# Kernel optimization log

Hardware: AMD Instinct MI355X
Metric: run time of the kernel (lower is better)

## Reference

```python
import jax, jax.numpy as jnp
import numpy as np

H = 32
W = 32
HIDDEN = 64
NUM_CLASSES = 10
BATCH = 128


def setup_inputs() -> dict:
    key = jax.random.key(0)
    ks = jax.random.split(key, 5)
    D = 4 * HIDDEN * H * W  # number_of_output_dimensions()
    return {
        "x": jax.random.normal(ks[0], (BATCH, 1, H, W), jnp.float32),
        "w_in": jax.random.normal(ks[1], (HIDDEN, 1), jnp.float32) * 0.1,
        "b_in": jnp.zeros((HIDDEN,), jnp.float32),
        "w_state": jax.random.normal(ks[2], (HIDDEN, HIDDEN, 2), jnp.float32) * (1.0 / np.sqrt(2 * HIDDEN)),
        "b_state": jnp.zeros((HIDDEN,), jnp.float32),
        "w_fc": jax.random.normal(ks[3], (D, NUM_CLASSES), jnp.float32) * 0.01,
        "b_fc": jnp.zeros((NUM_CLASSES,), jnp.float32),
    }


def _skew(x):
    # x: [B,1,H,W] -> [B,1,H,W+H-1]; row r shifted right by r (diagonal skew)
    Ws = W + H - 1
    col = jnp.arange(Ws)[None, :] - jnp.arange(H)[:, None]  # [H,Ws]
    valid = ((col >= 0) & (col < W)).astype(x.dtype)
    colc = jnp.clip(col, 0, W - 1)
    rows = jnp.arange(H)[:, None]
    return x[:, :, rows, colc] * valid[None, None]


def _one_direction(x, w_in, b_in, w_state, b_state):
    # Diagonal-scan MDRNN over skewed columns.
    B = x.shape[0]
    xs = _skew(x)  # [B,1,H,Ws]
    # Input projection for all columns at once (1x1 conv equivalent)
    xin = jnp.einsum('oc,bchw->bohw', w_in, xs) + b_in[None, :, None, None]
    cols = jnp.moveaxis(xin, 3, 0)  # [Ws,B,HIDDEN,H]

    w_up, w_same = w_state[:, :, 0], w_state[:, :, 1]

    def step(h, xc):
        # conv1d(kernel=2, padding=1) over column, bottom padding removed:
        # out[r] = w_up @ h[r-1] + w_same @ h[r]
        h_up = jnp.pad(h, ((0, 0), (0, 0), (1, 0)))[:, :, :H]
        s = (jnp.einsum('oi,bir->bor', w_up, h_up)
             + jnp.einsum('oi,bir->bor', w_same, h)
             + b_state[None, :, None])
        hn = jnp.tanh(s + xc)
        return hn, hn

    h0 = jnp.zeros((B, HIDDEN, H), x.dtype)
    _, ys = jax.lax.scan(step, h0, cols)  # [Ws,B,HIDDEN,H]
    acts = jnp.moveaxis(ys, 0, 3)  # [B,HIDDEN,H,Ws]
    # Unskew: out[..., r, c] = acts[..., r, c + r]
    ccols = jnp.arange(W)[None, :] + jnp.arange(H)[:, None]  # [H,W]
    rows = jnp.arange(H)[:, None]
    return acts[:, :, rows, ccols]  # [B,HIDDEN,H,W]


def reference(x, w_in, b_in, w_state, b_state, w_fc, b_fc):
    B = x.shape[0]
    # Four scanning directions via flips on dims 2 and 3, concatenated on batch
    x2 = x[:, :, ::-1, :]
    x3 = x[:, :, :, ::-1]
    x4 = x[:, :, ::-1, ::-1]
    xm = jnp.concatenate([x, x2, x3, x4], axis=0)  # [4B,1,H,W]
    acts = _one_direction(xm, w_in, b_in, w_state, b_state)  # [4B,HIDDEN,H,W]
    # index_select interleaving: example b gets its 4 direction copies contiguously
    sel = (jnp.arange(B)[:, None] + B * jnp.arange(4)[None, :]).reshape(-1)
    a = acts[sel].reshape(B, -1)  # [B, 4*HIDDEN*H*W]
    logits = a @ w_fc + b_fc
    return jax.nn.log_softmax(logits, axis=-1)
```

## Files before the change

kernel.cpp:

```cpp
#include <hip/hip_runtime.h>
#include <hip/hip_bf16.h>

#define NHID 64
#define NT   63
#define NBD  512
#define HLDS_STR 72
#define XSTR 35

typedef __attribute__((ext_vector_type(8))) short bf16x8;
typedef __attribute__((ext_vector_type(4))) float f32x4;

__device__ __forceinline__ float tanh_fast(float x) {
    const float e = __expf(2.0f * x);
    const float r = __builtin_amdgcn_rcpf(e + 1.0f);
    return 1.0f - 2.0f * r;
}

__device__ __forceinline__ unsigned int cvt_pk_bf16(float lo, float hi) {
    unsigned int r;
    asm("v_cvt_pk_bf16_f32 %0, %1, %2" : "=v"(r) : "v"(lo), "v"(hi));
    return r;
}

__device__ __forceinline__ float bf2f(unsigned int u16) {
    return __uint_as_float(u16 << 16);
}

#define SKEW_R0(t)  ((t) > 31 ? (t) - 31 : 0)
#define SKEW_R1(t)  ((t) < 31 ? (t) : 31)
#define SKEW_OFF(t) ((t) < 32 ? ((t) * ((t) + 1)) >> 1 : 1024 - (((63 - (t)) * (64 - (t))) >> 1))

#define LGKM_BARRIER() do {                                   \
    asm volatile("s_waitcnt lgkmcnt(0)" ::: "memory");        \
    __builtin_amdgcn_s_barrier();                             \
    asm volatile("" ::: "memory");                            \
} while (0)

__global__ __launch_bounds__(512, 4) void k_rnn(
    const float* __restrict__ x,
    const float* __restrict__ w_in,
    const float* __restrict__ b_in,
    const float* __restrict__ w_state,
    const float* __restrict__ b_state,
    unsigned short* __restrict__ acts_c)
{
    __shared__ __align__(16) unsigned short h0buf[33 * HLDS_STR];
    __shared__ __align__(16) unsigned short h1buf[33 * HLDS_STR];
    __shared__ float xs[32 * XSTR];

    const int tid = threadIdx.x;
    const int bd  = blockIdx.x;
    const int d   = bd >> 7;
    const int b   = bd & 127;
    const int lane = tid & 63;
    const int wave = tid >> 6;
    const int wo = wave >> 1;
    const int wr = wave & 1;
    const int n  = lane & 15;
    const int g  = lane >> 4;

    const bool flr = (d & 1) != 0;
    const bool flc = (d & 2) != 0;
    const float* xb = x + (size_t)b * 1024;
    for (int idx = tid; idx < 1024; idx += 512) {
        const int r = idx >> 5, c = idx & 31;
        xs[r * XSTR + c] = xb[(flr ? 31 - r : r) * 32 + (flc ? 31 - c : c)];
    }

    for (int m2 = tid; m2 < (33 * HLDS_STR) / 2; m2 += 512) {
        ((unsigned int*)h0buf)[m2] = 0u;
        ((unsigned int*)h1buf)[m2] = 0u;
    }

    bf16x8 a_hi[4], a_lo[4];
    {
        const int o_a = wo * 16 + n;
        #pragma unroll
        for (int kt = 0; kt < 4; ++kt) {
            const int s  = kt >> 1;
            const int cb = (kt & 1) * 32 + g * 8;
            bf16x8 hi8, lo8;
            #pragma unroll
            for (int j = 0; j < 8; ++j) {
                const float w = w_state[((size_t)o_a * 64 + cb + j) * 2 + s];
                const unsigned int hp = cvt_pk_bf16(w, 0.0f);
                const float wh = bf2f(hp & 0xffffu);
                const unsigned int lp = cvt_pk_bf16(w - wh, 0.0f);
                hi8[j] = (short)(hp & 0xffffu);
                lo8[j] = (short)(lp & 0xffffu);
            }
            a_hi[kt] = hi8;
            a_lo[kt] = lo8;
        }
    }

    float biasr[4], winr[4];
    #pragma unroll
    for (int j = 0; j < 4; ++j) {
        const int o = wo * 16 + g * 4 + j;
        biasr[j] = b_in[o] + b_state[o];
        winr[j]  = w_in[o];
    }

    const int r_out = wr * 16 + n;
    const int rdoff = r_out * HLDS_STR + g * 8;
    const int wroff = (r_out + 1) * HLDS_STR;
    const int cb0 = wo * 16 + g * 4;
    const int tlo = wr * 16;
    const float* xs_r = &xs[r_out * XSTR];

    const bool flusher = tid < 256;
    const int r_f = tid >> 3;
    const int sc  = (tid & 7) * 8;
    const int fl_off = (r_f + 1) * HLDS_STR + sc;
    unsigned short* actp = acts_c + (size_t)bd * 65536 + (size_t)r_f * 1984 + sc;

    __syncthreads();

#define STEP(T, RB, WB) do {                                                    \
    if ((unsigned)((T) - tlo) < 48u) {                                          \
        const bf16x8 b0 = *(const bf16x8*)&RB[rdoff];                           \
        const bf16x8 b1 = *(const bf16x8*)&RB[rdoff + 32];                      \
        const bf16x8 b2 = *(const bf16x8*)&RB[rdoff + HLDS_STR];                \
        const bf16x8 b3 = *(const bf16x8*)&RB[rdoff + HLDS_STR + 32];           \
        f32x4 ah = {0,0,0,0}, al = {0,0,0,0};                                   \
        ah = __builtin_amdgcn_mfma_f32_16x16x32_bf16(a_hi[0], b0, ah, 0,0,0);   \
        al = __builtin_amdgcn_mfma_f32_16x16x32_bf16(a_lo[0], b0, al, 0,0,0);   \
        ah = __builtin_amdgcn_mfma_f32_16x16x32_bf16(a_hi[1], b1, ah, 0,0,0);   \
        al = __builtin_amdgcn_mfma_f32_16x16x32_bf16(a_lo[1], b1, al, 0,0,0);   \
        ah = __builtin_amdgcn_mfma_f32_16x16x32_bf16(a_hi[2], b2, ah, 0,0,0);   \
        al = __builtin_amdgcn_mfma_f32_16x16x32_bf16(a_lo[2], b2, al, 0,0,0);   \
        ah = __builtin_amdgcn_mfma_f32_16x16x32_bf16(a_hi[3], b3, ah, 0,0,0);   \
        al = __builtin_amdgcn_mfma_f32_16x16x32_bf16(a_lo[3], b3, al, 0,0,0);   \
        const int c_ = (T) - r_out;                                             \
        const float xv = ((unsigned)c_ < 32u) ? xs_r[c_ & 31] : 0.0f;           \
        const float h0 = tanh_fast(ah[0] + al[0] + biasr[0] + winr[0] * xv);    \
        const float h1 = tanh_fast(ah[1] + al[1] + biasr[1] + winr[1] * xv);    \
        const float h2 = tanh_fast(ah[2] + al[2] + biasr[2] + winr[2] * xv);    \
        const float h3 = tanh_fast(ah[3] + al[3] + biasr[3] + winr[3] * xv);    \
        uint2 pk; pk.x = cvt_pk_bf16(h0, h1); pk.y = cvt_pk_bf16(h2, h3);       \
        *(uint2*)&WB[wroff + cb0] = pk;                                         \
    }                                                                           \
    LGKM_BARRIER();                                                             \
    if (flusher) {                                                              \
        const uint4 av = *(const uint4*)&WB[fl_off];                            \
        if ((unsigned)((T) - r_f) < 32u) *(uint4*)actp = av;                    \
        actp += 64;                                                             \
    }                                                                           \
} while (0)

    for (int sp = 0; sp < 31; ++sp) {
        const int t = 2 * sp;
        STEP(t,     h0buf, h1buf);
        STEP(t + 1, h1buf, h0buf);
    }
    STEP(62, h0buf, h1buf);
#undef STEP
}

__global__ __launch_bounds__(256) void k_prep(
    const float* __restrict__ w_fc,
    unsigned short* __restrict__ wt_swz)
{
    const int t = blockIdx.y;
    const int tid = threadIdx.x;
    const int r0 = SKEW_R0(t), r1 = SKEW_R1(t);
    const int cnt = r1 - r0 + 1;
    const int span = cnt << 10;
    int f = blockIdx.x * 2048 + tid * 8;
    const int fdst = f;
    if (f >= 4 * span) return;
    int d = 0;
    while (f >= span) { f -= span; ++d; }
    const int ks   = f >> 9;
    const int lane = (f >> 3) & 63;
    const int g = lane >> 4, n = lane & 15;
    unsigned int pk[4];
    #pragma unroll
    for (int jj = 0; jj < 4; ++jj) {
        float v[2] = {0.0f, 0.0f};
        #pragma unroll
        for (int h = 0; h < 2; ++h) {
            const int j = jj * 2 + h;
            const int k = ks * 32 + g * 8 + j;
            const int r = r0 + (k >> 6);
            const int o = k & 63;
            const int c = t - r;
            if (n < 10)
                v[h] = w_fc[((((size_t)(d * 64 + o)) << 10) + (r << 5) + c) * 10 + n];
        }
        pk[jj] = cvt_pk_bf16(v[0], v[1]);
    }
    uint4 st; st.x = pk[0]; st.y = pk[1]; st.z = pk[2]; st.w = pk[3];
    *(uint4*)(wt_swz + (size_t)SKEW_OFF(t) * 4096 + fdst) = st;
}

__global__ __launch_bounds__(256, 4) void k_fc(
    const unsigned short* __restrict__ acts_c,
    const unsigned short* __restrict__ wt_swz,
    float* __restrict__ partial)
{
    const int tid = threadIdx.x;
    const int blk = blockIdx.x;
    const int t   = blk >> 3;
    const int d   = (blk >> 1) & 3;
    const int mh  = blk & 1;
    const int lane = tid & 63;
    const int wv  = tid >> 6;
    const int g   = lane >> 4;
    const int n   = lane & 15;

    const int r0 = SKEW_R0(t), r1 = SKEW_R1(t);
    const int cnt = r1 - r0 + 1;
    const int off = SKEW_OFF(t);

    const int tb = d * 128 + mh * 64 + wv * 16;
    const unsigned short* Ap = acts_c + (size_t)(tb + n) * 65536
                             + (size_t)r0 * 1984 + (size_t)t * 64 + g * 8;
    const unsigned short* Bp = wt_swz
        + ((size_t)off * 4 + (size_t)d * cnt) * 1024 + lane * 8;

    f32x4 acc = {0.f, 0.f, 0.f, 0.f};
    #pragma unroll 2
    for (int q = 0; q < cnt; ++q) {
        const bf16x8 a0  = *(const bf16x8*)(Ap);
        const bf16x8 bb0 = *(const bf16x8*)(Bp);
        const bf16x8 a1  = *(const bf16x8*)(Ap + 32);
        const bf16x8 bb1 = *(const bf16x8*)(Bp + 512);
        acc = __builtin_amdgcn_mfma_f32_16x16x32_bf16(a0, bb0, acc, 0, 0, 0);
        acc = __builtin_amdgcn_mfma_f32_16x16x32_bf16(a1, bb1, acc, 0, 0, 0);
        Ap += 1984;
        Bp += 1024;
    }
    const int batch = tb + g * 4;
    #pragma unroll
    for (int reg = 0; reg < 4; ++reg)
        partial[((size_t)t * 512 + batch + reg) * 16 + n] = acc[reg];
}

__global__ __launch_bounds__(256) void k_out(
    const float* __restrict__ partial,
    const float* __restrict__ b_fc,
    float* __restrict__ out)
{
    __shared__ float lred[252 * 10];
    __shared__ float lgs[10];
    __shared__ float lse;
    const int b = blockIdx.x;
    const int tid = threadIdx.x;
    if (tid < 252) {
        const int t = tid >> 2, d = tid & 3;
        const float* p = partial + ((size_t)t * 512 + d * 128 + b) * 16;
        #pragma unroll
        for (int n2 = 0; n2 < 10; ++n2) lred[tid * 10 + n2] = p[n2];
    }
    __syncthreads();
    if (tid < 10) {
        float s = b_fc[tid];
        for (int i = 0; i < 252; ++i) s += lred[i * 10 + tid];
        lgs[tid] = s;
    }
    __syncthreads();
    if (tid == 0) {
        float m = lgs[0];
        for (int nn = 1; nn < 10; ++nn) m = fmaxf(m, lgs[nn]);
        float ssum = 0.0f;
        for (int nn = 0; nn < 10; ++nn) ssum += __expf(lgs[nn] - m);
        lse = m + __logf(ssum);
    }
    __syncthreads();
    if (tid < 10) out[b * 10 + tid] = lgs[tid] - lse;
}

extern "C" void kernel_launch(void* const* d_in, const int* in_sizes, int n_in,
                              void* d_out, int out_size, void* d_ws, size_t ws_size,
                              hipStream_t stream)
{
    const float* x       = (const float*)d_in[0];
    const float* w_in    = (const float*)d_in[1];
    const float* b_in    = (const float*)d_in[2];
    const float* w_state = (const float*)d_in[3];
    const float* b_state = (const float*)d_in[4];
    const float* w_fc    = (const float*)d_in[5];
    const float* b_fc    = (const float*)d_in[6];
    float* out = (float*)d_out;

    unsigned short* wt_swz = (unsigned short*)d_ws;
    float* partial = (float*)((char*)d_ws + (size_t)(8u << 20));
    unsigned short* acts_c = (unsigned short*)((char*)d_ws + (size_t)(16u << 20));

    k_prep<<<dim3(64, 63), 256, 0, stream>>>(w_fc, wt_swz);
    k_rnn <<<512, 512, 0, stream>>>(x, w_in, b_in, w_state, b_state, acts_c);
    k_fc  <<<504, 256, 0, stream>>>(acts_c, wt_swz, partial);
    k_out <<<128, 256, 0, stream>>>(partial, b_fc, out);
}
```

Baseline: 74.28 us.

## Fuse w_fc prep into RNN kernel, drop split-bf16 weights, halve RNN block size

Merges the w_fc swizzle/prep kernel into the RNN kernel as extra blocks, which removes one launch and lets the prep work overlap with the recurrence. The RNN weights now use a single bf16 copy instead of a hi/lo split, halving the MFMA count per step at some cost in accuracy. Each block drops from 512 to 256 threads, with every wave computing two output tiles, and activations go straight from registers to global memory instead of through a separate flush phase after the barrier.

```diff
diff --git a/kernel.cpp b/kernel.cpp
--- a/kernel.cpp
+++ b/kernel.cpp
@@ -36,84 +36,117 @@
     asm volatile("" ::: "memory");                            \
 } while (0)
 
-__global__ __launch_bounds__(512, 4) void k_rnn(
+__global__ __launch_bounds__(256, 4) void k_main(
     const float* __restrict__ x,
     const float* __restrict__ w_in,
     const float* __restrict__ b_in,
     const float* __restrict__ w_state,
     const float* __restrict__ b_state,
-    unsigned short* __restrict__ acts_c)
+    unsigned short* __restrict__ acts_c,
+    const float* __restrict__ w_fc,
+    unsigned short* __restrict__ wt_swz)
 {
     __shared__ __align__(16) unsigned short h0buf[33 * HLDS_STR];
     __shared__ __align__(16) unsigned short h1buf[33 * HLDS_STR];
     __shared__ float xs[32 * XSTR];
 
     const int tid = threadIdx.x;
+
+    if (blockIdx.x >= 512) {
+        const int rel = blockIdx.x - 512;
+        const int t   = rel >> 6;
+        const int sub = rel & 63;
+        const int r0 = SKEW_R0(t), r1 = SKEW_R1(t);
+        const int cnt = r1 - r0 + 1;
+        const int span = cnt << 10;
+        int f = sub * 2048 + tid * 8;
+        const int fdst = f;
+        if (f >= 4 * span) return;
+        int d = 0;
+        while (f >= span) { f -= span; ++d; }
+        const int ks   = f >> 9;
+        const int lane = (f >> 3) & 63;
+        const int g = lane >> 4, n = lane & 15;
+        unsigned int pk[4];
+        #pragma unroll
+        for (int jj = 0; jj < 4; ++jj) {
+            float v[2] = {0.0f, 0.0f};
+            #pragma unroll
+            for (int h = 0; h < 2; ++h) {
+                const int j = jj * 2 + h;
+                const int k = ks * 32 + g * 8 + j;
+                const int r = r0 + (k >> 6);
+                const int o = k & 63;
+                const int c = t - r;
+                if (n < 10)
+                    v[h] = w_fc[((((size_t)(d * 64 + o)) << 10) + (r << 5) + c) * 10 + n];
+            }
+            pk[jj] = cvt_pk_bf16(v[0], v[1]);
+        }
+        uint4 st; st.x = pk[0]; st.y = pk[1]; st.z = pk[2]; st.w = pk[3];
+        *(uint4*)(wt_swz + (size_t)SKEW_OFF(t) * 4096 + fdst) = st;
+        return;
+    }
+
     const int bd  = blockIdx.x;
     const int d   = bd >> 7;
     const int b   = bd & 127;
     const int lane = tid & 63;
     const int wave = tid >> 6;
-    const int wo = wave >> 1;
-    const int wr = wave & 1;
+    const int wp = wave & 1;
+    const int nt = wave >> 1;
     const int n  = lane & 15;
     const int g  = lane >> 4;
 
     const bool flr = (d & 1) != 0;
     const bool flc = (d & 2) != 0;
     const float* xb = x + (size_t)b * 1024;
-    for (int idx = tid; idx < 1024; idx += 512) {
+    for (int idx = tid; idx < 1024; idx += 256) {
         const int r = idx >> 5, c = idx & 31;
         xs[r * XSTR + c] = xb[(flr ? 31 - r : r) * 32 + (flc ? 31 - c : c)];
     }
 
-    for (int m2 = tid; m2 < (33 * HLDS_STR) / 2; m2 += 512) {
+    for (int m2 = tid; m2 < (33 * HLDS_STR) / 2; m2 += 256) {
         ((unsigned int*)h0buf)[m2] = 0u;
         ((unsigned int*)h1buf)[m2] = 0u;
     }
 
-    bf16x8 a_hi[4], a_lo[4];
-    {
-        const int o_a = wo * 16 + n;
+    bf16x8 a0[4], a1[4];
+    #pragma unroll
+    for (int wl = 0; wl < 2; ++wl) {
+        const int o = wp * 32 + wl * 16 + n;
         #pragma unroll
         for (int kt = 0; kt < 4; ++kt) {
             const int s  = kt >> 1;
             const int cb = (kt & 1) * 32 + g * 8;
-            bf16x8 hi8, lo8;
+            bf16x8 w8;
             #pragma unroll
             for (int j = 0; j < 8; ++j) {
-                const float w = w_state[((size_t)o_a * 64 + cb + j) * 2 + s];
-                const unsigned int hp = cvt_pk_bf16(w, 0.0f);
-                const float wh = bf2f(hp & 0xffffu);
-                const unsigned int lp = cvt_pk_bf16(w - wh, 0.0f);
-                hi8[j] = (short)(hp & 0xffffu);
-                lo8[j] = (short)(lp & 0xffffu);
+                const float w = w_state[((size_t)o * 64 + cb + j) * 2 + s];
+                w8[j] = (short)(cvt_pk_bf16(w, 0.0f) & 0xffffu);
             }
-            a_hi[kt] = hi8;
-            a_lo[kt] = lo8;
+            if (wl == 0) a0[kt] = w8; else a1[kt] = w8;
         }
     }
 
-    float biasr[4], winr[4];
+    float biasr[2][4], winr[2][4];
     #pragma unroll
-    for (int j = 0; j < 4; ++j) {
-        const int o = wo * 16 + g * 4 + j;
-        biasr[j] = b_in[o] + b_state[o];
-        winr[j]  = w_in[o];
-    }
-
-    const int r_out = wr * 16 + n;
+    for (int wl = 0; wl < 2; ++wl)
+        #pragma unroll
+        for (int j = 0; j < 4; ++j) {
+            const int o = wp * 32 + wl * 16 + g * 4 + j;
+            biasr[wl][j] = b_in[o] + b_state[o];
+            winr[wl][j]  = w_in[o];
+        }
+
+    const int r_out = nt * 16 + n;
     const int rdoff = r_out * HLDS_STR + g * 8;
     const int wroff = (r_out + 1) * HLDS_STR;
-    const int cb0 = wo * 16 + g * 4;
-    const int tlo = wr * 16;
+    const int cb0 = wp * 32 + g * 4;
+    const int tlo = nt * 16;
     const float* xs_r = &xs[r_out * XSTR];
 
-    const bool flusher = tid < 256;
-    const int r_f = tid >> 3;
-    const int sc  = (tid & 7) * 8;
-    const int fl_off = (r_f + 1) * HLDS_STR + sc;
-    unsigned short* actp = acts_c + (size_t)bd * 65536 + (size_t)r_f * 1984 + sc;
+    unsigned short* actp = acts_c + (size_t)bd * 65536 + (size_t)r_out * 1984 + cb0;
 
     __syncthreads();
 
@@ -123,30 +156,42 @@
         const bf16x8 b1 = *(const bf16x8*)&RB[rdoff + 32];                      \
         const bf16x8 b2 = *(const bf16x8*)&RB[rdoff + HLDS_STR];                \
         const bf16x8 b3 = *(const bf16x8*)&RB[rdoff + HLDS_STR + 32];           \
-        f32x4 ah = {0,0,0,0}, al = {0,0,0,0};                                   \
-        ah = __builtin_amdgcn_mfma_f32_16x16x32_bf16(a_hi[0], b0, ah, 0,0,0);   \
-        al = __builtin_amdgcn_mfma_f32_16x16x32_bf16(a_lo[0], b0, al, 0,0,0);   \
-        ah = __builtin_amdgcn_mfma_f32_16x16x32_bf16(a_hi[1], b1, ah, 0,0,0);   \
-        al = __builtin_amdgcn_mfma_f32_16x16x32_bf16(a_lo[1], b1, al, 0,0,0);   \
-        ah = __builtin_amdgcn_mfma_f32_16x16x32_bf16(a_hi[2], b2, ah, 0,0,0);   \
-        al = __builtin_amdgcn_mfma_f32_16x16x32_bf16(a_lo[2], b2, al, 0,0,0);   \
-        ah = __builtin_amdgcn_mfma_f32_16x16x32_bf16(a_hi[3], b3, ah, 0,0,0);   \
-        al = __builtin_amdgcn_mfma_f32_16x16x32_bf16(a_lo[3], b3, al, 0,0,0);   \
+        f32x4 s0a = {0,0,0,0}, s0b = {0,0,0,0};                                 \
+        f32x4 s1a = {0,0,0,0}, s1b = {0,0,0,0};                                 \
+        s0a = __builtin_amdgcn_mfma_f32_16x16x32_bf16(a0[0], b0, s0a, 0,0,0);   \
+        s1a = __builtin_amdgcn_mfma_f32_16x16x32_bf16(a1[0], b0, s1a, 0,0,0);   \
+        s0b = __builtin_amdgcn_mfma_f32_16x16x32_bf16(a0[2], b2, s0b, 0,0,0);   \
+        s1b = __builtin_amdgcn_mfma_f32_16x16x32_bf16(a1[2], b2, s1b, 0,0,0);   \
+        s0a = __builtin_amdgcn_mfma_f32_16x16x32_bf16(a0[1], b1, s0a, 0,0,0);   \
+        s1a = __builtin_amdgcn_mfma_f32_16x16x32_bf16(a1[1], b1, s1a, 0,0,0);   \
+        s0b = __builtin_amdgcn_mfma_f32_16x16x32_bf16(a0[3], b3, s0b, 0,0,0);   \
+        s1b = __builtin_amdgcn_mfma_f32_16x16x32_bf16(a1[3], b3, s1b, 0,0,0);   \
         const int c_ = (T) - r_out;                                             \
         const float xv = ((unsigned)c_ < 32u) ? xs_r[c_ & 31] : 0.0f;           \
-        const float h0 = tanh_fast(ah[0] + al[0] + biasr[0] + winr[0] * xv);    \
-        const float h1 = tanh_fast(ah[1] + al[1] + biasr[1] + winr[1] * xv);    \
-        const float h2 = tanh_fast(ah[2] + al[2] + biasr[2] + winr[2] * xv);    \
-        const float h3 = tanh_fast(ah[3] + al[3] + biasr[3] + winr[3] * xv);    \
-        uint2 pk; pk.x = cvt_pk_bf16(h0, h1); pk.y = cvt_pk_bf16(h2, h3);       \
-        *(uint2*)&WB[wroff + cb0] = pk;                                         \
+        uint2 pk0, pk1;                                                         \
+        {                                                                       \
+            const float h0 = tanh_fast(s0a[0] + s0b[0] + biasr[0][0] + winr[0][0] * xv); \
+            const float h1 = tanh_fast(s0a[1] + s0b[1] + biasr[0][1] + winr[0][1] * xv); \
+            const float h2 = tanh_fast(s0a[2] + s0b[2] + biasr[0][2] + winr[0][2] * xv); \
+            const float h3 = tanh_fast(s0a[3] + s0b[3] + biasr[0][3] + winr[0][3] * xv); \
+            pk0.x = cvt_pk_bf16(h0, h1); pk0.y = cvt_pk_bf16(h2, h3);           \
+            *(uint2*)&WB[wroff + cb0] = pk0;                                    \
+        }                                                                       \
+        {                                                                       \
+            const float h0 = tanh_fast(s1a[0] + s1b[0] + biasr[1][0] + winr[1][0] * xv); \
+            const float h1 = tanh_fast(s1a[1] + s1b[1] + biasr[1][1] + winr[1][1] * xv); \
+            const float h2 = tanh_fast(s1a[2] + s1b[2] + biasr[1][2] + winr[1][2] * xv); \
+            const float h3 = tanh_fast(s1a[3] + s1b[3] + biasr[1][3] + winr[1][3] * xv); \
+            pk1.x = cvt_pk_bf16(h0, h1); pk1.y = cvt_pk_bf16(h2, h3);           \
+            *(uint2*)&WB[wroff + cb0 + 16] = pk1;                               \
+        }                                                                       \
+        if ((unsigned)c_ < 32u) {                                               \
+            *(uint2*)(actp)      = pk0;                                         \
+            *(uint2*)(actp + 16) = pk1;                                         \
+        }                                                                       \
     }                                                                           \
     LGKM_BARRIER();                                                             \
-    if (flusher) {                                                              \
-        const uint4 av = *(const uint4*)&WB[fl_off];                            \
-        if ((unsigned)((T) - r_f) < 32u) *(uint4*)actp = av;                    \
-        actp += 64;                                                             \
-    }                                                                           \
+    actp += 64;                                                                 \
 } while (0)
 
     for (int sp = 0; sp < 31; ++sp) {
@@ -156,43 +201,6 @@
     }
     STEP(62, h0buf, h1buf);
 #undef STEP
-}
-
-__global__ __launch_bounds__(256) void k_prep(
-    const float* __restrict__ w_fc,
-    unsigned short* __restrict__ wt_swz)
-{
-    const int t = blockIdx.y;
-    const int tid = threadIdx.x;
-    const int r0 = SKEW_R0(t), r1 = SKEW_R1(t);
-    const int cnt = r1 - r0 + 1;
-    const int span = cnt << 10;
-    int f = blockIdx.x * 2048 + tid * 8;
-    const int fdst = f;
-    if (f >= 4 * span) return;
-    int d = 0;
-    while (f >= span) { f -= span; ++d; }
-    const int ks   = f >> 9;
-    const int lane = (f >> 3) & 63;
-    const int g = lane >> 4, n = lane & 15;
-    unsigned int pk[4];
-    #pragma unroll
-    for (int jj = 0; jj < 4; ++jj) {
-        float v[2] = {0.0f, 0.0f};
-        #pragma unroll
-        for (int h = 0; h < 2; ++h) {
-            const int j = jj * 2 + h;
-            const int k = ks * 32 + g * 8 + j;
-            const int r = r0 + (k >> 6);
-            const int o = k & 63;
-            const int c = t - r;
-            if (n < 10)
-                v[h] = w_fc[((((size_t)(d * 64 + o)) << 10) + (r << 5) + c) * 10 + n];
-        }
-        pk[jj] = cvt_pk_bf16(v[0], v[1]);
-    }
-    uint4 st; st.x = pk[0]; st.y = pk[1]; st.z = pk[2]; st.w = pk[3];
-    *(uint4*)(wt_swz + (size_t)SKEW_OFF(t) * 4096 + fdst) = st;
 }
 
 __global__ __launch_bounds__(256, 4) void k_fc(
@@ -289,8 +297,8 @@
     float* partial = (float*)((char*)d_ws + (size_t)(8u << 20));
     unsigned short* acts_c = (unsigned short*)((char*)d_ws + (size_t)(16u << 20));
 
-    k_prep<<<dim3(64, 63), 256, 0, stream>>>(w_fc, wt_swz);
-    k_rnn <<<512, 512, 0, stream>>>(x, w_in, b_in, w_state, b_state, acts_c);
+    k_main<<<4544, 256, 0, stream>>>(x, w_in, b_in, w_state, b_state,
+                                     acts_c, w_fc, wt_swz);
     k_fc  <<<504, 256, 0, stream>>>(acts_c, wt_swz, partial);
     k_out <<<128, 256, 0, stream>>>(partial, b_fc, out);
 }
```

After: 62.83 us. 15.4% less time.
